# Optimization experiments

Hardware: AMD Instinct MI355X
Metric: run time of the kernel (lower is better)

Reference implementation:

```python
import jax, jax.numpy as jnp
import numpy as np

B, S, D, H, O = 8, 4096, 512, 512, 512
NS, NC, SD = 4, 4, 8
CLIP, TEMP, SUP_SCALE, SUP_EPS, LN_EPS = 3.0, 1.0, 1.0, 1e-4, 1e-5


def _ln(x, w, b):
    m = jnp.mean(x, -1, keepdims=True)
    v = jnp.mean((x - m) ** 2, -1, keepdims=True)
    return (x - m) * jax.lax.rsqrt(v + LN_EPS) * w + b


def _lin(x, w, b):
    return x @ w.T + b


def setup_inputs() -> dict:
    key = jax.random.key(0)
    ks = iter(jax.random.split(key, 32))

    def W(shape):
        return 0.02 * jax.random.normal(next(ks), shape, jnp.float32)

    inp = {}
    inp['x'] = jax.random.normal(next(ks), (B, S, D), jnp.float32)
    inp['sb_norm_w'] = jnp.ones((D,), jnp.float32)
    inp['sb_norm_b'] = jnp.zeros((D,), jnp.float32)
    inp['sb_proj_w'] = W((NS, D)); inp['sb_proj_b'] = jnp.zeros((NS,), jnp.float32)
    inp['sb_sum_w'] = W((SD, 4)); inp['sb_sum_b'] = jnp.zeros((SD,), jnp.float32)
    inp['cb_norm_w'] = jnp.ones((D,), jnp.float32)
    inp['cb_norm_b'] = jnp.zeros((D,), jnp.float32)
    inp['cb_proj_w'] = W((NC, D)); inp['cb_proj_b'] = jnp.zeros((NC,), jnp.float32)
    inp['cb_sum_w'] = W((SD, 4)); inp['cb_sum_b'] = jnp.zeros((SD,), jnp.float32)
    inp['vn_norm_w'] = jnp.ones((D,), jnp.float32)
    inp['vn_norm_b'] = jnp.zeros((D,), jnp.float32)
    inp['vn_w1'] = W((H, D)); inp['vn_b1'] = jnp.zeros((H,), jnp.float32)
    inp['vn_w2'] = W((O, H)); inp['vn_b2'] = jnp.zeros((O,), jnp.float32)
    inp['un_norm_w'] = jnp.ones((D,), jnp.float32)
    inp['un_norm_b'] = jnp.zeros((D,), jnp.float32)
    inp['un_w1'] = W((H, D)); inp['un_b1'] = jnp.zeros((H,), jnp.float32)
    inp['un_w2'] = W((1, H)); inp['un_b2'] = jnp.zeros((1,), jnp.float32)
    inp['en_w'] = W((H, 1)); inp['en_b'] = jnp.zeros((H,), jnp.float32)
    inp['pr_w'] = W((H, 1)); inp['pr_b'] = jnp.zeros((H,), jnp.float32)
    inp['rs_w'] = W((H, 1)); inp['rs_b'] = jnp.zeros((H,), jnp.float32)
    inp['ssp_w'] = W((H, SD)); inp['ssp_b'] = jnp.zeros((H,), jnp.float32)
    inp['csp_w'] = W((H, SD)); inp['csp_b'] = jnp.zeros((H,), jnp.float32)
    inp['out_w'] = W((O, O + 5 * H)); inp['out_b'] = jnp.zeros((O,), jnp.float32)
    inp['support_logits'] = jnp.zeros((NS,), jnp.float32)
    inp['conflict_weights'] = jnp.ones((NC,), jnp.float32)
    inp['drive_bias'] = jnp.zeros((1,), jnp.float32)
    inp['bias_resistance'] = jnp.zeros((1,), jnp.float32)
    inp['update_threshold'] = jnp.ones((1,), jnp.float32)
    inp['eml_gamma'] = jnp.full((1,), 0.3, jnp.float32)
    inp['eml_lambda'] = jnp.ones((1,), jnp.float32)
    inp['eml_bias'] = jnp.zeros((1,), jnp.float32)
    return inp


def reference(x, sb_norm_w, sb_norm_b, sb_proj_w, sb_proj_b, sb_sum_w, sb_sum_b,
              cb_norm_w, cb_norm_b, cb_proj_w, cb_proj_b, cb_sum_w, cb_sum_b,
              vn_norm_w, vn_norm_b, vn_w1, vn_b1, vn_w2, vn_b2,
              un_norm_w, un_norm_b, un_w1, un_b1, un_w2, un_b2,
              en_w, en_b, pr_w, pr_b, rs_w, rs_b,
              ssp_w, ssp_b, csp_w, csp_b, out_w, out_b,
              support_logits, conflict_weights, drive_bias, bias_resistance,
              update_threshold, eml_gamma, eml_lambda, eml_bias):
    # Support bank: LN -> Linear -> softplus(+eps) -> stats -> summary Linear
    sf = jax.nn.softplus(_lin(_ln(x, sb_norm_w, sb_norm_b), sb_proj_w, sb_proj_b)) + SUP_EPS  # [B,S,NS]
    ls = jnp.log(sf)
    s_seed = jnp.concatenate([
        sf.mean(-1, keepdims=True), sf.std(-1, keepdims=True),
        ls.mean(-1, keepdims=True), ls.max(-1, keepdims=True)], -1)
    ss = _lin(s_seed, sb_sum_w, sb_sum_b)  # [B,S,SD]
    # Conflict bank
    cf = jax.nn.softplus(_lin(_ln(x, cb_norm_w, cb_norm_b), cb_proj_w, cb_proj_b))  # [B,S,NC]
    c_seed = jnp.concatenate([
        cf.mean(-1, keepdims=True), cf.std(-1, keepdims=True),
        cf.max(-1, keepdims=True), cf.min(-1, keepdims=True)], -1)
    cs = _lin(c_seed, cb_sum_w, cb_sum_b)  # [B,S,SD]
    # Drive / resistance
    sw = jax.nn.softmax(support_logits)
    drive = drive_bias + SUP_SCALE * (ls * sw).sum(-1, keepdims=True) / np.sqrt(NS)
    cw = jax.nn.softplus(conflict_weights)
    weighted_conflict = (cf * cw).sum(-1, keepdims=True) / np.sqrt(NC)
    u_h = jax.nn.gelu(_lin(_ln(x, un_norm_w, un_norm_b), un_w1, un_b1), approximate=False)
    uncertainty = jax.nn.softplus(_lin(u_h, un_w2, un_b2))  # [B,S,1]
    resistance = bias_resistance + weighted_conflict + uncertainty
    # EML unit (dim=1): bounded linear drive-resistance balance, warmup_eta=1.0
    e_raw = eml_gamma * drive - eml_lambda * resistance + eml_bias
    energy = CLIP * jnp.tanh(e_raw / CLIP)
    activation = jax.nn.sigmoid(energy / TEMP)
    precision = jax.nn.softplus(energy - update_threshold)
    # Value net
    v_h = jax.nn.gelu(_lin(_ln(x, vn_norm_w, vn_norm_b), vn_w1, vn_b1), approximate=False)
    value = _lin(v_h, vn_w2, vn_b2)  # [B,S,O]
    feats = jnp.concatenate([
        activation * value,
        _lin(energy, en_w, en_b),
        _lin(precision, pr_w, pr_b),
        _lin(resistance, rs_w, rs_b),
        _lin(ss, ssp_w, ssp_b),
        _lin(cs, csp_w, csp_b)], -1)  # [B,S,O+5H]
    return _lin(feats, out_w, out_b)  # [B,S,O]
```

## Files before the change

kernel.cpp:

```cpp
#include <hip/hip_runtime.h>
#include <stdint.h>

typedef unsigned short u16;
typedef __bf16 bf16x8 __attribute__((ext_vector_type(8)));
typedef float f32x4 __attribute__((ext_vector_type(4)));
typedef __attribute__((address_space(1))) void gvoid;
typedef __attribute__((address_space(3))) void lvoid;

#define NTOK 32768

__device__ __forceinline__ u16 f2bf(float f) {
    unsigned u = __float_as_uint(f);
    u += 0x7fffu + ((u >> 16) & 1u);
    return (u16)(u >> 16);
}
__device__ __forceinline__ float softplusf(float x) {
    return fmaxf(x, 0.f) + log1pf(expf(-fabsf(x)));
}
__device__ __forceinline__ float geluf(float x) {
    return 0.5f * x * (1.f + erff(x * 0.7071067811865475f));
}
__device__ __forceinline__ float wave_sum(float v) {
#pragma unroll
    for (int o = 32; o > 0; o >>= 1) v += __shfl_xor(v, o);
    return v;
}
__device__ __forceinline__ float blk_sum(float v) {
    __shared__ float sm[4];
    v = wave_sum(v);
    __syncthreads();
    if ((threadIdx.x & 63) == 0) sm[threadIdx.x >> 6] = v;
    __syncthreads();
    return sm[0] + sm[1] + sm[2] + sm[3];
}

__global__ void k_fold(
    const float* __restrict__ vnw1, const float* __restrict__ vnnw, const float* __restrict__ vnnb, const float* __restrict__ vnb1,
    const float* __restrict__ unw1, const float* __restrict__ unnw, const float* __restrict__ unnb, const float* __restrict__ unb1,
    const float* __restrict__ sbpw, const float* __restrict__ sbpb, const float* __restrict__ sbnw, const float* __restrict__ sbnb,
    const float* __restrict__ cbpw, const float* __restrict__ cbpb, const float* __restrict__ cbnw, const float* __restrict__ cbnb,
    const float* __restrict__ outw, const float* __restrict__ enw, const float* __restrict__ enb,
    const float* __restrict__ prw, const float* __restrict__ prb,
    const float* __restrict__ rsw, const float* __restrict__ rsb,
    const float* __restrict__ sspw, const float* __restrict__ sspb,
    const float* __restrict__ cspw, const float* __restrict__ cspb,
    const float* __restrict__ vnw2, const float* __restrict__ vnb2,
    u16* __restrict__ Astk, float* __restrict__ bstk, float* __restrict__ pb,
    u16* __restrict__ Aow, u16* __restrict__ vnT,
    float* __restrict__ a_en, float* __restrict__ a_pr, float* __restrict__ a_rs,
    float* __restrict__ b_vo, float* __restrict__ c_cn, float* __restrict__ Mss, float* __restrict__ Mcs)
{
    const int b = blockIdx.x, t = threadIdx.x;
    if (b < 1024) {
        const float *w1, *nw, *nb; float bias;
        if (b < 512) { w1 = vnw1 + (size_t)b * 512; nw = vnnw; nb = vnnb; bias = vnb1[b]; }
        else { int r = b - 512; w1 = unw1 + (size_t)r * 512; nw = unnw; nb = unnb; bias = unb1[r]; }
        float part = 0.f;
        for (int d = t; d < 512; d += 256) {
            float wv = w1[d];
            Astk[(size_t)b * 512 + d] = f2bf(wv * nw[d]);
            part += wv * nb[d];
        }
        float s = blk_sum(part);
        if (t == 0) bstk[b] = bias + s;
    } else if (b < 1032) {
        int j = b - 1024;
        const float *pw, *nw, *nb; float bias;
        if (j < 4) { pw = sbpw + j * 512; nw = sbnw; nb = sbnb; bias = sbpb[j]; }
        else { pw = cbpw + (j - 4) * 512; nw = cbnw; nb = cbnb; bias = cbpb[j - 4]; }
        float part = 0.f;
        for (int d = t; d < 512; d += 256) {
            float wv = pw[d];
            Astk[(size_t)(1024 + j) * 512 + d] = f2bf(wv * nw[d]);
            part += wv * nb[d];
        }
        float s = blk_sum(part);
        if (t == 0) pb[j] = bias + s;
    } else if (b < 1152) {
        for (int d = t; d < 512; d += 256) Astk[(size_t)b * 512 + d] = 0;
    } else if (b < 1664) {
        int i = b - 1152;
        const float* ow = outw + (size_t)i * 3072;
        float pen = 0, ppr = 0, prs = 0, pbv = 0, pcc = 0;
        float pms[8], pmc[8];
#pragma unroll
        for (int k = 0; k < 8; k++) { pms[k] = 0.f; pmc[k] = 0.f; }
        for (int h = t; h < 512; h += 256) {
            float o0 = ow[h];        Aow[(size_t)i * 512 + h] = f2bf(o0); pbv += o0 * vnb2[h];
            float o1 = ow[512 + h];  pen += o1 * enw[h]; pcc += o1 * enb[h];
            float o2 = ow[1024 + h]; ppr += o2 * prw[h]; pcc += o2 * prb[h];
            float o3 = ow[1536 + h]; prs += o3 * rsw[h]; pcc += o3 * rsb[h];
            float o4 = ow[2048 + h]; pcc += o4 * sspb[h];
            float o5 = ow[2560 + h]; pcc += o5 * cspb[h];
#pragma unroll
            for (int k = 0; k < 8; k++) { pms[k] += o4 * sspw[h * 8 + k]; pmc[k] += o5 * cspw[h * 8 + k]; }
        }
        float r;
        r = blk_sum(pen); if (t == 0) a_en[i] = r;
        r = blk_sum(ppr); if (t == 0) a_pr[i] = r;
        r = blk_sum(prs); if (t == 0) a_rs[i] = r;
        r = blk_sum(pbv); if (t == 0) b_vo[i] = r;
        r = blk_sum(pcc); if (t == 0) c_cn[i] = r;
        for (int k = 0; k < 8; k++) { r = blk_sum(pms[k]); if (t == 0) Mss[i * 8 + k] = r; }
        for (int k = 0; k < 8; k++) { r = blk_sum(pmc[k]); if (t == 0) Mcs[i * 8 + k] = r; }
    } else {
        int hrow = b - 1664;
        for (int o = t; o < 512; o += 256)
            vnT[(size_t)hrow * 512 + o] = f2bf(vnw2[(size_t)o * 512 + hrow]);
    }
}

__device__ __forceinline__ void gt_stage(const u16* __restrict__ A_, int lda,
                                         const u16* __restrict__ B_, int ldb, int kt,
                                         u16* dA, u16* dB, int w, int lrow, int lcol)
{
#pragma unroll
    for (int i = 0; i < 4; i++) {
        const int chunk = i * 4 + w;
        const int row = chunk * 8 + lrow;
        __builtin_amdgcn_global_load_lds((gvoid*)const_cast<u16*>(A_ + (size_t)row * lda + kt + lcol),
                                         (lvoid*)(dA + chunk * 512), 16, 0, 0);
        __builtin_amdgcn_global_load_lds((gvoid*)const_cast<u16*>(B_ + (size_t)row * ldb + kt + lcol),
                                         (lvoid*)(dB + chunk * 512), 16, 0, 0);
    }
}

__device__ __forceinline__ void gt_compute(const u16* lA, const u16* lB, f32x4 (&acc)[4][4],
                                           int wr, int wc, int frow, int fk, int sw)
{
#pragma unroll
    for (int ks = 0; ks < 2; ks++) {
        bf16x8 af[4], bfv[4];
        const int c = (ks * 32 + fk);
#pragma unroll
        for (int rt = 0; rt < 4; rt++)
            af[rt] = *(const bf16x8*)(lA + (wr + rt * 16 + frow) * 64 + (c ^ sw));
#pragma unroll
        for (int ct = 0; ct < 4; ct++)
            bfv[ct] = *(const bf16x8*)(lB + (wc + ct * 16 + frow) * 64 + (c ^ sw));
#pragma unroll
        for (int rt = 0; rt < 4; rt++)
#pragma unroll
            for (int ct = 0; ct < 4; ct++)
                acc[rt][ct] = __builtin_amdgcn_mfma_f32_16x16x32_bf16(af[rt], bfv[ct], acc[rt][ct], 0, 0, 0);
    }
}

__device__ __forceinline__ void gemm_tile(const u16* __restrict__ Ab, int lda,
                                          const u16* __restrict__ Bb, int ldb,
                                          int K, u16* sm, f32x4 (&acc)[4][4])
{
    const int t = threadIdx.x;
    const int w = t >> 6, l = t & 63;
    const int lrow = l >> 3;
    const int lcol = ((l ^ (((l >> 3) & 3) << 1)) & 7) * 8;
    const int wr = ((w >> 1) << 6), wc = ((w & 1) << 6);
    const int frow = l & 15, fk = ((l >> 4) << 3);
    const int sw = (frow & 3) << 4;
    u16* lA0 = sm;          u16* lA1 = sm + 8192;
    u16* lB0 = sm + 16384;  u16* lB1 = sm + 24576;

    gt_stage(Ab, lda, Bb, ldb, 0, lA0, lB0, w, lrow, lcol);
    __syncthreads();
    for (int kt = 0; kt < K; kt += 128) {
        if (kt + 64 < K) gt_stage(Ab, lda, Bb, ldb, kt + 64, lA1, lB1, w, lrow, lcol);
        gt_compute(lA0, lB0, acc, wr, wc, frow, fk, sw);
        __syncthreads();
        if (kt + 128 < K) gt_stage(Ab, lda, Bb, ldb, kt + 128, lA0, lB0, w, lrow, lcol);
        gt_compute(lA1, lB1, acc, wr, wc, frow, fk, sw);
        __syncthreads();
    }
}

__global__ __launch_bounds__(256, 2) void k_gemm_wvo(const u16* __restrict__ A, const u16* __restrict__ Bm,
                                                     u16* __restrict__ C)
{
    __shared__ __align__(16) u16 smem[32768];
    const f32x4 zero = {0.f, 0.f, 0.f, 0.f};
    f32x4 acc[4][4];
#pragma unroll
    for (int a = 0; a < 4; a++)
#pragma unroll
        for (int c = 0; c < 4; c++) acc[a][c] = zero;
    const u16* Ab = A + (size_t)blockIdx.y * 128 * 512;
    const u16* Bb = Bm + (size_t)blockIdx.x * 128 * 512;
    gemm_tile(Ab, 512, Bb, 512, 512, smem, acc);
    const int t = threadIdx.x, w = t >> 6, l = t & 63;
    const int rbase = blockIdx.y * 128 + ((w >> 1) << 6);
    const int cbase = blockIdx.x * 128 + ((w & 1) << 6);
    const int lr = ((l >> 4) << 2), lc = l & 15;
#pragma unroll
    for (int rt = 0; rt < 4; rt++)
#pragma unroll
        for (int ct = 0; ct < 4; ct++)
#pragma unroll
            for (int j = 0; j < 4; j++)
                C[(size_t)(rbase + rt * 16 + lr + j) * 512 + cbase + ct * 16 + lc] = f2bf(acc[rt][ct][j]);
}

__global__ void k_token(const float* __restrict__ x, u16* __restrict__ Ybf)
{
    const int w = threadIdx.x >> 6, l = threadIdx.x & 63;
    const int n = blockIdx.x * 4 + w;
    const float* xr = x + (size_t)n * 512;
    float4 xa = *(const float4*)(xr + 4 * l);
    float4 xb = *(const float4*)(xr + 256 + 4 * l);
    float v[8] = {xa.x, xa.y, xa.z, xa.w, xb.x, xb.y, xb.z, xb.w};
    float s1 = 0.f, s2 = 0.f;
#pragma unroll
    for (int c = 0; c < 8; c++) { s1 += v[c]; s2 += v[c] * v[c]; }
    s1 = wave_sum(s1); s2 = wave_sum(s2);
    const float mean = s1 * (1.f / 512.f);
    const float var = s2 * (1.f / 512.f) - mean * mean;
    const float rstd = rsqrtf(var + 1e-5f);
    float y[8];
#pragma unroll
    for (int c = 0; c < 8; c++) y[c] = (v[c] - mean) * rstd;
    *(ushort4*)(Ybf + (size_t)n * 512 + 4 * l) = make_ushort4(f2bf(y[0]), f2bf(y[1]), f2bf(y[2]), f2bf(y[3]));
    *(ushort4*)(Ybf + (size_t)n * 512 + 256 + 4 * l) = make_ushort4(f2bf(y[4]), f2bf(y[5]), f2bf(y[6]), f2bf(y[7]));
}

__global__ __launch_bounds__(256, 2) void k_gemm1(const u16* __restrict__ Y, const u16* __restrict__ Ast,
                                                  const float* __restrict__ bstk, const float* __restrict__ pb,
                                                  const float* __restrict__ unw2,
                                                  u16* __restrict__ H, float* __restrict__ wp,
                                                  float* __restrict__ wdotp)
{
    __shared__ __align__(16) u16 smem[32768];
    const f32x4 zero = {0.f, 0.f, 0.f, 0.f};
    f32x4 acc[4][4];
#pragma unroll
    for (int a = 0; a < 4; a++)
#pragma unroll
        for (int c = 0; c < 4; c++) acc[a][c] = zero;
    const int nwg = gridDim.x * gridDim.y;
    const int lin = blockIdx.y * gridDim.x + blockIdx.x;
    const int swz = (lin & 7) * (nwg >> 3) + (lin >> 3);
    const int by = swz / gridDim.x, bx = swz % gridDim.x;
    const u16* Ab = Y + (size_t)by * 128 * 512;
    const u16* Bb = Ast + (size_t)bx * 128 * 512;
    gemm_tile(Ab, 512, Bb, 512, 512, smem, acc);
    const int t = threadIdx.x, w = t >> 6, l = t & 63;
    const int wr = ((w >> 1) << 6), wc = ((w & 1) << 6);
    const int lr = ((l >> 4) << 2), lc = l & 15;
    if (bx == 8) {
        if ((w & 1) == 0 && lc < 8) {
            const float bv = pb[lc];
            const int rbase = by * 128 + wr;
#pragma unroll
            for (int rt = 0; rt < 4; rt++)
#pragma unroll
                for (int j = 0; j < 4; j++) {
                    const int n = rbase + rt * 16 + lr + j;
                    wp[(size_t)n * 8 + lc] = acc[rt][0][j] + bv;
                }
        }
        return;
    }
    if (bx >= 4) {
        const int cb = (bx - 4) * 128;
        float part[4][4];
#pragma unroll
        for (int rt = 0; rt < 4; rt++)
#pragma unroll
            for (int j = 0; j < 4; j++) part[rt][j] = 0.f;
#pragma unroll
        for (int ct = 0; ct < 4; ct++) {
            const int col = cb + wc + ct * 16 + lc;
            const float bv = bstk[512 + col];
            const float w2 = unw2[col];
#pragma unroll
            for (int rt = 0; rt < 4; rt++)
#pragma unroll
                for (int j = 0; j < 4; j++)
                    part[rt][j] += geluf(acc[rt][ct][j] + bv) * w2;
        }
        float* sf = (float*)smem;
        const int slot = ((w & 1) << 4) | lc;
        __syncthreads();
#pragma unroll
        for (int rt = 0; rt < 4; rt++)
#pragma unroll
            for (int j = 0; j < 4; j++)
                sf[(wr + rt * 16 + lr + j) * 32 + slot] = part[rt][j];
        __syncthreads();
        if (t < 128) {
            float s = 0.f;
#pragma unroll
            for (int k2 = 0; k2 < 32; k2++) s += sf[t * 32 + k2];
            wdotp[(size_t)(bx - 4) * NTOK + by * 128 + t] = s;
        }
        return;
    }
#pragma unroll
    for (int ct = 0; ct < 4; ct++) {
        const int col = wc + ct * 16 + lc;
        const float bv = bstk[bx * 128 + col];
#pragma unroll
        for (int rt = 0; rt < 4; rt++) {
            const int row = wr + rt * 16 + lr;
#pragma unroll
            for (int j = 0; j < 4; j++)
                smem[(row + j) * 136 + col] = f2bf(geluf(acc[rt][ct][j] + bv));
        }
    }
    __syncthreads();
    const size_t gbase = (size_t)(by * 128) * 512 + bx * 128;
#pragma unroll
    for (int jj = 0; jj < 8; jj++) {
        const int r = jj * 16 + (t >> 4), u = t & 15;
        bf16x8 vv = *(const bf16x8*)(smem + r * 136 + u * 8);
        *(bf16x8*)(H + gbase + (size_t)r * 512 + u * 8) = vv;
    }
}

__global__ void k_bank(const float* __restrict__ wp, const float* __restrict__ wdotp,
                       const float* __restrict__ unb2,
                       const float* __restrict__ sbsw, const float* __restrict__ sbsb,
                       const float* __restrict__ cbsw, const float* __restrict__ cbsb,
                       const float* __restrict__ suplog, const float* __restrict__ confw,
                       const float* __restrict__ drvb, const float* __restrict__ biasres,
                       const float* __restrict__ emlg, const float* __restrict__ emll,
                       const float* __restrict__ emlb, const float* __restrict__ updthr,
                       float* __restrict__ wss, float* __restrict__ wcs, float* __restrict__ wsc)
{
    const int n = blockIdx.x * 256 + threadIdx.x;
    float4 p0 = *(const float4*)(wp + (size_t)n * 8);
    float4 p1 = *(const float4*)(wp + (size_t)n * 8 + 4);
    float p[8] = {p0.x, p0.y, p0.z, p0.w, p1.x, p1.y, p1.z, p1.w};
    const float dot = wdotp[n] + wdotp[NTOK + n] + wdotp[2 * NTOK + n] + wdotp[3 * NTOK + n];
    float sf[4], lsv[4], cf[4];
#pragma unroll
    for (int j = 0; j < 4; j++) {
        sf[j] = softplusf(p[j]) + 1e-4f;
        lsv[j] = logf(sf[j]);
        cf[j] = softplusf(p[j + 4]);
    }
    const float smn = 0.25f * (sf[0] + sf[1] + sf[2] + sf[3]);
    float sd = 0.f;
#pragma unroll
    for (int j = 0; j < 4; j++) sd += (sf[j] - smn) * (sf[j] - smn);
    const float sstd = sqrtf(0.25f * sd);
    const float lmn = 0.25f * (lsv[0] + lsv[1] + lsv[2] + lsv[3]);
    const float lmx = fmaxf(fmaxf(lsv[0], lsv[1]), fmaxf(lsv[2], lsv[3]));
    const float cmn = 0.25f * (cf[0] + cf[1] + cf[2] + cf[3]);
    float cd = 0.f;
#pragma unroll
    for (int j = 0; j < 4; j++) cd += (cf[j] - cmn) * (cf[j] - cmn);
    const float cstd = sqrtf(0.25f * cd);
    const float cmx = fmaxf(fmaxf(cf[0], cf[1]), fmaxf(cf[2], cf[3]));
    const float cmi = fminf(fminf(cf[0], cf[1]), fminf(cf[2], cf[3]));
    float seed_s[4] = {smn, sstd, lmn, lmx};
    float seed_c[4] = {cmn, cstd, cmx, cmi};
    float a4[8], b4[8];
#pragma unroll
    for (int k = 0; k < 8; k++) {
        float a = sbsb[k], b2 = cbsb[k];
#pragma unroll
        for (int j = 0; j < 4; j++) { a += sbsw[k * 4 + j] * seed_s[j]; b2 += cbsw[k * 4 + j] * seed_c[j]; }
        a4[k] = a; b4[k] = b2;
    }
    *(float4*)(wss + (size_t)n * 8)     = make_float4(a4[0], a4[1], a4[2], a4[3]);
    *(float4*)(wss + (size_t)n * 8 + 4) = make_float4(a4[4], a4[5], a4[6], a4[7]);
    *(float4*)(wcs + (size_t)n * 8)     = make_float4(b4[0], b4[1], b4[2], b4[3]);
    *(float4*)(wcs + (size_t)n * 8 + 4) = make_float4(b4[4], b4[5], b4[6], b4[7]);
    float mx = fmaxf(fmaxf(suplog[0], suplog[1]), fmaxf(suplog[2], suplog[3]));
    float e[4], se = 0.f;
#pragma unroll
    for (int j = 0; j < 4; j++) { e[j] = expf(suplog[j] - mx); se += e[j]; }
    float dv = 0.f, wcv = 0.f;
#pragma unroll
    for (int j = 0; j < 4; j++) { dv += lsv[j] * (e[j] / se); wcv += cf[j] * softplusf(confw[j]); }
    const float drive = drvb[0] + 0.5f * dv;
    const float unc = softplusf(dot + unb2[0]);
    const float res = biasres[0] + 0.5f * wcv + unc;
    const float er = emlg[0] * drive - emll[0] * res + emlb[0];
    const float energy = 3.f * tanhf(er * (1.f / 3.f));
    const float act = 1.f / (1.f + expf(-energy));
    const float prc = softplusf(energy - updthr[0]);
    wsc[(size_t)n * 4 + 0] = act;
    wsc[(size_t)n * 4 + 1] = energy;
    wsc[(size_t)n * 4 + 2] = prc;
    wsc[(size_t)n * 4 + 3] = res;
}

__global__ __launch_bounds__(256, 2) void k_gemm2(const u16* __restrict__ H, const u16* __restrict__ Wvo,
    const float* __restrict__ wsc, const float* __restrict__ wss, const float* __restrict__ wcs,
    const float* __restrict__ a_en, const float* __restrict__ a_pr, const float* __restrict__ a_rs,
    const float* __restrict__ b_vo, const float* __restrict__ c_cn,
    const float* __restrict__ Mss, const float* __restrict__ Mcs,
    const float* __restrict__ outb, float* __restrict__ out)
{
    __shared__ __align__(16) u16 smem[32768];
    const f32x4 zero = {0.f, 0.f, 0.f, 0.f};
    f32x4 acc[4][4];
#pragma unroll
    for (int a = 0; a < 4; a++)
#pragma unroll
        for (int c = 0; c < 4; c++) acc[a][c] = zero;
    const int nwg = gridDim.x * gridDim.y;
    const int lin = blockIdx.y * gridDim.x + blockIdx.x;
    const int swz = (lin & 7) * (nwg >> 3) + (lin >> 3);
    const int by = swz / gridDim.x, bx = swz % gridDim.x;
    const u16* Ab = H + (size_t)by * 128 * 512;
    const u16* Bb = Wvo + (size_t)bx * 128 * 512;
    gemm_tile(Ab, 512, Bb, 512, 512, smem, acc);
    const int t = threadIdx.x, w = t >> 6, l = t & 63;
    const int rbase = by * 128 + ((w >> 1) << 6);
    const int cbase = bx * 128 + ((w & 1) << 6);
    const int lr = ((l >> 4) << 2), lc = l & 15;
    float bvo4[4], aen4[4], apr4[4], ars4[4], cc4[4], ms4[4][8], mc4[4][8];
#pragma unroll
    for (int ct = 0; ct < 4; ct++) {
        const int i = cbase + ct * 16 + lc;
        bvo4[ct] = b_vo[i]; aen4[ct] = a_en[i]; apr4[ct] = a_pr[i]; ars4[ct] = a_rs[i];
        cc4[ct] = c_cn[i] + outb[i];
#pragma unroll
        for (int k = 0; k < 8; k++) { ms4[ct][k] = Mss[i * 8 + k]; mc4[ct][k] = Mcs[i * 8 + k]; }
    }
#pragma unroll
    for (int rt = 0; rt < 4; rt++)
#pragma unroll
        for (int j = 0; j < 4; j++) {
            const int n = rbase + rt * 16 + lr + j;
            const float act = wsc[(size_t)n * 4 + 0];
            const float eng = wsc[(size_t)n * 4 + 1];
            const float prc = wsc[(size_t)n * 4 + 2];
            const float res = wsc[(size_t)n * 4 + 3];
            float sv[8], cv[8];
#pragma unroll
            for (int k = 0; k < 8; k++) { sv[k] = wss[(size_t)n * 8 + k]; cv[k] = wcs[(size_t)n * 8 + k]; }
#pragma unroll
            for (int ct = 0; ct < 4; ct++) {
                const int i = cbase + ct * 16 + lc;
                float o = act * (acc[rt][ct][j] + bvo4[ct]) + eng * aen4[ct] + prc * apr4[ct]
                        + res * ars4[ct] + cc4[ct];
#pragma unroll
                for (int k = 0; k < 8; k++) o += ms4[ct][k] * sv[k] + mc4[ct][k] * cv[k];
                out[(size_t)n * 512 + i] = o;
            }
        }
}

extern "C" void kernel_launch(void* const* d_in, const int* in_sizes, int n_in,
                              void* d_out, int out_size, void* d_ws, size_t ws_size,
                              hipStream_t stream)
{
    const float* x       = (const float*)d_in[0];
    const float* sbnw    = (const float*)d_in[1];
    const float* sbnb    = (const float*)d_in[2];
    const float* sbpw    = (const float*)d_in[3];
    const float* sbpb    = (const float*)d_in[4];
    const float* sbsw    = (const float*)d_in[5];
    const float* sbsb    = (const float*)d_in[6];
    const float* cbnw    = (const float*)d_in[7];
    const float* cbnb    = (const float*)d_in[8];
    const float* cbpw    = (const float*)d_in[9];
    const float* cbpb    = (const float*)d_in[10];
    const float* cbsw    = (const float*)d_in[11];
    const float* cbsb    = (const float*)d_in[12];
    const float* vnnw    = (const float*)d_in[13];
    const float* vnnb    = (const float*)d_in[14];
    const float* vnw1    = (const float*)d_in[15];
    const float* vnb1    = (const float*)d_in[16];
    const float* vnw2    = (const float*)d_in[17];
    const float* vnb2    = (const float*)d_in[18];
    const float* unnw    = (const float*)d_in[19];
    const float* unnb    = (const float*)d_in[20];
    const float* unw1    = (const float*)d_in[21];
    const float* unb1    = (const float*)d_in[22];
    const float* unw2    = (const float*)d_in[23];
    const float* unb2    = (const float*)d_in[24];
    const float* enw     = (const float*)d_in[25];
    const float* enb     = (const float*)d_in[26];
    const float* prw     = (const float*)d_in[27];
    const float* prb     = (const float*)d_in[28];
    const float* rsw     = (const float*)d_in[29];
    const float* rsb     = (const float*)d_in[30];
    const float* sspw    = (const float*)d_in[31];
    const float* sspb    = (const float*)d_in[32];
    const float* cspw    = (const float*)d_in[33];
    const float* cspb    = (const float*)d_in[34];
    const float* outw    = (const float*)d_in[35];
    const float* outb    = (const float*)d_in[36];
    const float* suplog  = (const float*)d_in[37];
    const float* confw   = (const float*)d_in[38];
    const float* drvb    = (const float*)d_in[39];
    const float* biasres = (const float*)d_in[40];
    const float* updthr  = (const float*)d_in[41];
    const float* emlg    = (const float*)d_in[42];
    const float* emll    = (const float*)d_in[43];
    const float* emlb    = (const float*)d_in[44];
    float* out = (float*)d_out;
    (void)in_sizes; (void)n_in; (void)out_size; (void)ws_size;

    char* wsp = (char*)d_ws;
    size_t off = 0;
    auto alloc = [&](size_t bytes) { char* p = wsp + off; off = (off + bytes + 255) & ~(size_t)255; return p; };
    u16*  Ybf  = (u16*)alloc((size_t)NTOK * 512 * 2);
    u16*  Hbf  = (u16*)alloc((size_t)NTOK * 512 * 2);
    u16*  Astk = (u16*)alloc(1152 * 512 * 2);
    float* bstk = (float*)alloc(1024 * 4);
    float* pb   = (float*)alloc(8 * 4);
    u16*  Aow  = (u16*)alloc(512 * 512 * 2);
    u16*  vnT  = (u16*)alloc(512 * 512 * 2);
    u16*  Wvo  = (u16*)alloc(512 * 512 * 2);
    float* a_en = (float*)alloc(512 * 4);
    float* a_pr = (float*)alloc(512 * 4);
    float* a_rs = (float*)alloc(512 * 4);
    float* b_vo = (float*)alloc(512 * 4);
    float* c_cn = (float*)alloc(512 * 4);
    float* Mss  = (float*)alloc(512 * 8 * 4);
    float* Mcs  = (float*)alloc(512 * 8 * 4);
    float* wp   = (float*)alloc((size_t)NTOK * 8 * 4);
    float* wdotp= (float*)alloc((size_t)NTOK * 4 * 4);
    float* wss  = (float*)alloc((size_t)NTOK * 8 * 4);
    float* wcs  = (float*)alloc((size_t)NTOK * 8 * 4);
    float* wsc  = (float*)alloc((size_t)NTOK * 4 * 4);

    k_fold<<<2176, 256, 0, stream>>>(vnw1, vnnw, vnnb, vnb1, unw1, unnw, unnb, unb1,
                                     sbpw, sbpb, sbnw, sbnb, cbpw, cbpb, cbnw, cbnb,
                                     outw, enw, enb, prw, prb, rsw, rsb, sspw, sspb, cspw, cspb,
                                     vnw2, vnb2,
                                     Astk, bstk, pb, Aow, vnT, a_en, a_pr, a_rs, b_vo, c_cn, Mss, Mcs);
    k_gemm_wvo<<<dim3(4, 4), 256, 0, stream>>>(Aow, vnT, Wvo);
    k_token<<<NTOK / 4, 256, 0, stream>>>(x, Ybf);
    k_gemm1<<<dim3(9, 256), 256, 0, stream>>>(Ybf, Astk, bstk, pb, unw2, Hbf, wp, wdotp);
    k_bank<<<NTOK / 256, 256, 0, stream>>>(wp, wdotp, unb2, sbsw, sbsb, cbsw, cbsb,
                                           suplog, confw, drvb, biasres, emlg, emll, emlb, updthr,
                                           wss, wcs, wsc);
    k_gemm2<<<dim3(4, 256), 256, 0, stream>>>(Hbf, Wvo, wsc, wss, wcs, a_en, a_pr, a_rs, b_vo, c_cn,
                                              Mss, Mcs, outb, out);
}
```

Before: 154.9 us.

## Switch GEMMs to 256x256 tiles with 8-wave pipelined mainloop

Replaces the 128x128, 4-wave GEMM tiles in k_gemm1 and k_gemm2 with 256x256 tiles computed by 512-thread blocks. A new mainloop issues staged global-to-LDS loads split by quadrant, with explicit vmcnt waits, barriers and raised wave priority around the MFMA bursts. The stacked weight matrix is padded to 1280 rows so the bank projection fits in a fifth tile column, and the uncertainty partial dot shrinks from four partials to two. Larger tiles cut redundant global loads and raise arithmetic intensity, but they need 128KB of LDS and many accumulator registers, leave fewer blocks, and waste padded rows in the bank tile.

Result: slower. 530.1 us (+242.3%).

```diff
diff --git a/kernel.cpp b/kernel.cpp
--- a/kernel.cpp
+++ b/kernel.cpp
@@ -8,6 +8,11 @@
 typedef __attribute__((address_space(3))) void lvoid;
 
 #define NTOK 32768
+
+#define FENCE() asm volatile("" ::: "memory")
+#define SBAR()  do { FENCE(); __builtin_amdgcn_s_barrier(); FENCE(); } while (0)
+#define SVM6()  asm volatile("s_waitcnt vmcnt(6)" ::: "memory")
+#define SVM0()  asm volatile("s_waitcnt vmcnt(0)" ::: "memory")
 
 __device__ __forceinline__ u16 f2bf(float f) {
     unsigned u = __float_as_uint(f);
@@ -76,10 +81,10 @@
         }
         float s = blk_sum(part);
         if (t == 0) pb[j] = bias + s;
-    } else if (b < 1152) {
+    } else if (b < 1280) {
         for (int d = t; d < 512; d += 256) Astk[(size_t)b * 512 + d] = 0;
-    } else if (b < 1664) {
-        int i = b - 1152;
+    } else if (b < 1792) {
+        int i = b - 1280;
         const float* ow = outw + (size_t)i * 3072;
         float pen = 0, ppr = 0, prs = 0, pbv = 0, pcc = 0;
         float pms[8], pmc[8];
@@ -104,9 +109,109 @@
         for (int k = 0; k < 8; k++) { r = blk_sum(pms[k]); if (t == 0) Mss[i * 8 + k] = r; }
         for (int k = 0; k < 8; k++) { r = blk_sum(pmc[k]); if (t == 0) Mcs[i * 8 + k] = r; }
     } else {
-        int hrow = b - 1664;
+        int hrow = b - 1792;
         for (int o = t; o < 512; o += 256)
             vnT[(size_t)hrow * 512 + o] = f2bf(vnw2[(size_t)o * 512 + hrow]);
+    }
+}
+
+__device__ __forceinline__ void load_bfrag(const u16* bufB, bf16x8 (&bfrag)[4][2], int wn, int l) {
+#pragma unroll
+    for (int nt = 0; nt < 4; nt++) {
+        const int row = wn * 64 + nt * 16 + (l & 15);
+#pragma unroll
+        for (int ks = 0; ks < 2; ks++) {
+            const int s = (ks * 4 + (l >> 4)) ^ (row & 7);
+            bfrag[nt][ks] = *(const bf16x8*)(bufB + row * 64 + (s << 3));
+        }
+    }
+}
+
+template <int Q>
+__device__ __forceinline__ void load_aquad(const u16* bufA, bf16x8 (&af)[2][2], int wm, int l) {
+#pragma unroll
+    for (int m2 = 0; m2 < 2; m2++) {
+        const int row = (Q * 2 + m2) * 32 + wm * 16 + (l & 15);
+#pragma unroll
+        for (int ks = 0; ks < 2; ks++) {
+            const int s = (ks * 4 + (l >> 4)) ^ (row & 7);
+            af[m2][ks] = *(const bf16x8*)(bufA + row * 64 + (s << 3));
+        }
+    }
+}
+
+template <int Q>
+__device__ __forceinline__ void do_mfma(bf16x8 (&af)[2][2], bf16x8 (&bfrag)[4][2], f32x4 (&acc)[8][4]) {
+#pragma unroll
+    for (int m2 = 0; m2 < 2; m2++)
+#pragma unroll
+        for (int nt = 0; nt < 4; nt++)
+#pragma unroll
+            for (int ks = 0; ks < 2; ks++)
+                acc[Q * 2 + m2][nt] =
+                    __builtin_amdgcn_mfma_f32_16x16x32_bf16(af[m2][ks], bfrag[nt][ks], acc[Q * 2 + m2][nt], 0, 0, 0);
+}
+
+#define PHASE(Q, bufA_, bufB_, READB, STAGE_STMT, VM_STMT)        \
+    do {                                                          \
+        if (READB) load_bfrag(bufB_, bfrag, wn, l);               \
+        bf16x8 af[2][2];                                          \
+        load_aquad<Q>(bufA_, af, wm, l);                          \
+        STAGE_STMT;                                               \
+        SBAR();                                                   \
+        __builtin_amdgcn_s_setprio(1);                            \
+        do_mfma<Q>(af, bfrag, acc);                               \
+        __builtin_amdgcn_s_setprio(0);                            \
+        VM_STMT;                                                  \
+        SBAR();                                                   \
+    } while (0)
+
+__device__ __forceinline__ void gemm8_mainloop(const u16* __restrict__ Ag, const u16* __restrict__ Bg,
+                                               size_t arow0, size_t brow0,
+                                               u16* sm, f32x4 (&acc)[8][4], int w, int l)
+{
+    const int wm = w >> 2, wn = w & 3;
+    u16* const sA0 = sm;
+    u16* const sA1 = sm + 16384;
+    u16* const sB0 = sm + 32768;
+    u16* const sB1 = sm + 49152;
+    const int rchunk = l >> 3;
+    const int gc = (((l & 7) ^ (l >> 3)) << 3);
+
+    auto STG = [&](const u16* g, size_t rb, int tile, int half, u16* lbase) {
+        const int kt = tile * 64;
+#pragma unroll
+        for (int i = 0; i < 2; i++) {
+            const int r0 = half * 128 + (w * 2 + i) * 8;
+            __builtin_amdgcn_global_load_lds(
+                (gvoid*)const_cast<u16*>(g + (rb + r0 + rchunk) * 512 + kt + gc),
+                (lvoid*)(lbase + r0 * 64), 16, 0, 0);
+        }
+    };
+
+    STG(Ag, arow0, 0, 0, sA0);
+    STG(Ag, arow0, 0, 1, sA0);
+    STG(Bg, brow0, 0, 0, sB0);
+    STG(Bg, brow0, 0, 1, sB0);
+    STG(Bg, brow0, 1, 0, sB1);
+    STG(Ag, arow0, 1, 0, sA1);
+    STG(Bg, brow0, 1, 1, sB1);
+    SVM6();
+    SBAR();
+
+    bf16x8 bfrag[4][2];
+    for (int it = 0; it < 4; ++it) {
+        const int t1 = 2 * it + 1, t2 = 2 * it + 2, t3 = 2 * it + 3;
+        const bool lastit = (it == 3);
+        PHASE(0, sA0, sB0, true,  { STG(Ag, arow0, t1, 1, sA1); }, );
+        PHASE(1, sA0, sB0, false, { if (t2 < 8) STG(Bg, brow0, t2, 0, sB0); }, );
+        PHASE(2, sA0, sB0, false, { if (t2 < 8) STG(Ag, arow0, t2, 0, sA0); }, );
+        PHASE(3, sA0, sB0, false, { if (t2 < 8) STG(Bg, brow0, t2, 1, sB0); },
+              { if (lastit) { SVM0(); } else { SVM6(); } });
+        PHASE(0, sA1, sB1, true,  { if (t2 < 8) STG(Ag, arow0, t2, 1, sA0); }, );
+        PHASE(1, sA1, sB1, false, { if (t3 < 8) STG(Bg, brow0, t3, 0, sB1); }, );
+        PHASE(2, sA1, sB1, false, { if (t3 < 8) STG(Ag, arow0, t3, 0, sA1); }, );
+        PHASE(3, sA1, sB1, false, { if (t3 < 8) STG(Bg, brow0, t3, 1, sB1); }, { SVM6(); });
     }
 }
 
@@ -124,7 +229,6 @@
                                          (lvoid*)(dB + chunk * 512), 16, 0, 0);
     }
 }
-
 __device__ __forceinline__ void gt_compute(const u16* lA, const u16* lB, f32x4 (&acc)[4][4],
                                            int wr, int wc, int frow, int fk, int sw)
 {
@@ -145,7 +249,6 @@
                 acc[rt][ct] = __builtin_amdgcn_mfma_f32_16x16x32_bf16(af[rt], bfv[ct], acc[rt][ct], 0, 0, 0);
     }
 }
-
 __device__ __forceinline__ void gemm_tile(const u16* __restrict__ Ab, int lda,
                                           const u16* __restrict__ Bb, int ldb,
                                           int K, u16* sm, f32x4 (&acc)[4][4])
@@ -159,7 +262,6 @@
     const int sw = (frow & 3) << 4;
     u16* lA0 = sm;          u16* lA1 = sm + 8192;
     u16* lB0 = sm + 16384;  u16* lB1 = sm + 24576;
-
     gt_stage(Ab, lda, Bb, ldb, 0, lA0, lB0, w, lrow, lcol);
     __syncthreads();
     for (int kt = 0; kt < K; kt += 128) {
@@ -220,97 +322,90 @@
     *(ushort4*)(Ybf + (size_t)n * 512 + 256 + 4 * l) = make_ushort4(f2bf(y[4]), f2bf(y[5]), f2bf(y[6]), f2bf(y[7]));
 }
 
-__global__ __launch_bounds__(256, 2) void k_gemm1(const u16* __restrict__ Y, const u16* __restrict__ Ast,
+__global__ __launch_bounds__(512, 2) void k_gemm1(const u16* __restrict__ Y, const u16* __restrict__ Ast,
                                                   const float* __restrict__ bstk, const float* __restrict__ pb,
                                                   const float* __restrict__ unw2,
                                                   u16* __restrict__ H, float* __restrict__ wp,
                                                   float* __restrict__ wdotp)
 {
-    __shared__ __align__(16) u16 smem[32768];
-    const f32x4 zero = {0.f, 0.f, 0.f, 0.f};
-    f32x4 acc[4][4];
-#pragma unroll
-    for (int a = 0; a < 4; a++)
-#pragma unroll
-        for (int c = 0; c < 4; c++) acc[a][c] = zero;
+    __shared__ __align__(16) u16 smem[65536];
+    f32x4 acc[8][4];
+#pragma unroll
+    for (int a = 0; a < 8; a++)
+#pragma unroll
+        for (int c = 0; c < 4; c++) acc[a][c] = (f32x4){0.f, 0.f, 0.f, 0.f};
     const int nwg = gridDim.x * gridDim.y;
     const int lin = blockIdx.y * gridDim.x + blockIdx.x;
     const int swz = (lin & 7) * (nwg >> 3) + (lin >> 3);
     const int by = swz / gridDim.x, bx = swz % gridDim.x;
-    const u16* Ab = Y + (size_t)by * 128 * 512;
-    const u16* Bb = Ast + (size_t)bx * 128 * 512;
-    gemm_tile(Ab, 512, Bb, 512, 512, smem, acc);
-    const int t = threadIdx.x, w = t >> 6, l = t & 63;
-    const int wr = ((w >> 1) << 6), wc = ((w & 1) << 6);
-    const int lr = ((l >> 4) << 2), lc = l & 15;
-    if (bx == 8) {
-        if ((w & 1) == 0 && lc < 8) {
-            const float bv = pb[lc];
-            const int rbase = by * 128 + wr;
-#pragma unroll
-            for (int rt = 0; rt < 4; rt++)
+    const int tid = threadIdx.x, w = tid >> 6, l = tid & 63;
+    const int wm = w >> 2, wn = w & 3;
+
+    gemm8_mainloop(Y, Ast, (size_t)by * 256, (size_t)bx * 256, smem, acc, w, l);
+
+    if (bx >= 4) {
+        if (wn == 0 && (l & 15) < 8) {
+            const float bv = pb[l & 15];
+#pragma unroll
+            for (int mt = 0; mt < 8; mt++)
 #pragma unroll
                 for (int j = 0; j < 4; j++) {
-                    const int n = rbase + rt * 16 + lr + j;
-                    wp[(size_t)n * 8 + lc] = acc[rt][0][j] + bv;
+                    const int n = by * 256 + mt * 32 + wm * 16 + ((l >> 4) << 2) + j;
+                    wp[(size_t)n * 8 + (l & 15)] = acc[mt][0][j] + bv;
                 }
         }
         return;
     }
-    if (bx >= 4) {
-        const int cb = (bx - 4) * 128;
-        float part[4][4];
-#pragma unroll
-        for (int rt = 0; rt < 4; rt++)
-#pragma unroll
-            for (int j = 0; j < 4; j++) part[rt][j] = 0.f;
-#pragma unroll
-        for (int ct = 0; ct < 4; ct++) {
-            const int col = cb + wc + ct * 16 + lc;
-            const float bv = bstk[512 + col];
-            const float w2 = unw2[col];
-#pragma unroll
-            for (int rt = 0; rt < 4; rt++)
-#pragma unroll
-                for (int j = 0; j < 4; j++)
-                    part[rt][j] += geluf(acc[rt][ct][j] + bv) * w2;
-        }
+    if (bx >= 2) {
         float* sf = (float*)smem;
-        const int slot = ((w & 1) << 4) | lc;
+#pragma unroll
+        for (int mt = 0; mt < 8; mt++)
+#pragma unroll
+            for (int j = 0; j < 4; j++) {
+                float ps = 0.f;
+#pragma unroll
+                for (int nt = 0; nt < 4; nt++) {
+                    const int c = wn * 64 + nt * 16 + (l & 15);
+                    const int ui = (bx - 2) * 256 + c;
+                    ps += geluf(acc[mt][nt][j] + bstk[512 + ui]) * unw2[ui];
+                }
+                const int row = mt * 32 + wm * 16 + ((l >> 4) << 2) + j;
+                sf[row * 65 + wn * 16 + (l & 15)] = ps;
+            }
         __syncthreads();
-#pragma unroll
-        for (int rt = 0; rt < 4; rt++)
-#pragma unroll
-            for (int j = 0; j < 4; j++)
-                sf[(wr + rt * 16 + lr + j) * 32 + slot] = part[rt][j];
+        if (tid < 256) {
+            float s = 0.f;
+#pragma unroll
+            for (int c = 0; c < 64; c++) s += sf[tid * 65 + c];
+            wdotp[(size_t)(bx - 2) * NTOK + by * 256 + tid] = s;
+        }
+        return;
+    }
+#pragma unroll
+    for (int p = 0; p < 2; p++) {
+#pragma unroll
+        for (int m2 = 0; m2 < 4; m2++) {
+            const int mt = p * 4 + m2;
+#pragma unroll
+            for (int nt = 0; nt < 4; nt++) {
+                const int c = wn * 64 + nt * 16 + (l & 15);
+                const float bv = bstk[bx * 256 + c];
+#pragma unroll
+                for (int j = 0; j < 4; j++) {
+                    const int rloc = mt * 32 + wm * 16 + ((l >> 4) << 2) + j - p * 128;
+                    smem[rloc * 264 + c] = f2bf(geluf(acc[mt][nt][j] + bv));
+                }
+            }
+        }
         __syncthreads();
-        if (t < 128) {
-            float s = 0.f;
-#pragma unroll
-            for (int k2 = 0; k2 < 32; k2++) s += sf[t * 32 + k2];
-            wdotp[(size_t)(bx - 4) * NTOK + by * 128 + t] = s;
-        }
-        return;
-    }
-#pragma unroll
-    for (int ct = 0; ct < 4; ct++) {
-        const int col = wc + ct * 16 + lc;
-        const float bv = bstk[bx * 128 + col];
-#pragma unroll
-        for (int rt = 0; rt < 4; rt++) {
-            const int row = wr + rt * 16 + lr;
-#pragma unroll
-            for (int j = 0; j < 4; j++)
-                smem[(row + j) * 136 + col] = f2bf(geluf(acc[rt][ct][j] + bv));
-        }
-    }
-    __syncthreads();
-    const size_t gbase = (size_t)(by * 128) * 512 + bx * 128;
-#pragma unroll
-    for (int jj = 0; jj < 8; jj++) {
-        const int r = jj * 16 + (t >> 4), u = t & 15;
-        bf16x8 vv = *(const bf16x8*)(smem + r * 136 + u * 8);
-        *(bf16x8*)(H + gbase + (size_t)r * 512 + u * 8) = vv;
+        const int r = tid >> 5, u = tid & 31;
+#pragma unroll
+        for (int s = 0; s < 8; s++) {
+            const int rr = s * 16 + r;
+            bf16x8 vv = *(const bf16x8*)(smem + rr * 264 + u * 8);
+            *(bf16x8*)(H + (size_t)(by * 256 + p * 128 + rr) * 512 + bx * 256 + u * 8) = vv;
+        }
+        __syncthreads();
     }
 }
 
@@ -328,7 +423,7 @@
     float4 p0 = *(const float4*)(wp + (size_t)n * 8);
     float4 p1 = *(const float4*)(wp + (size_t)n * 8 + 4);
     float p[8] = {p0.x, p0.y, p0.z, p0.w, p1.x, p1.y, p1.z, p1.w};
-    const float dot = wdotp[n] + wdotp[NTOK + n] + wdotp[2 * NTOK + n] + wdotp[3 * NTOK + n];
+    const float dot = wdotp[n] + wdotp[NTOK + n];
     float sf[4], lsv[4], cf[4];
 #pragma unroll
     for (int j = 0; j < 4; j++) {
@@ -384,62 +479,66 @@
     wsc[(size_t)n * 4 + 3] = res;
 }
 
-__global__ __launch_bounds__(256, 2) void k_gemm2(const u16* __restrict__ H, const u16* __restrict__ Wvo,
+__global__ __launch_bounds__(512, 2) void k_gemm2(const u16* __restrict__ H, const u16* __restrict__ Wvo,
     const float* __restrict__ wsc, const float* __restrict__ wss, const float* __restrict__ wcs,
     const float* __restrict__ a_en, const float* __restrict__ a_pr, const float* __restrict__ a_rs,
     const float* __restrict__ b_vo, const float* __restrict__ c_cn,
     const float* __restrict__ Mss, const float* __restrict__ Mcs,
     const float* __restrict__ outb, float* __restrict__ out)
 {
-    __shared__ __align__(16) u16 smem[32768];
-    const f32x4 zero = {0.f, 0.f, 0.f, 0.f};
-    f32x4 acc[4][4];
-#pragma unroll
-    for (int a = 0; a < 4; a++)
-#pragma unroll
-        for (int c = 0; c < 4; c++) acc[a][c] = zero;
+    __shared__ __align__(16) u16 smem[65536];
+    f32x4 acc[8][4];
+#pragma unroll
+    for (int a = 0; a < 8; a++)
+#pragma unroll
+        for (int c = 0; c < 4; c++) acc[a][c] = (f32x4){0.f, 0.f, 0.f, 0.f};
     const int nwg = gridDim.x * gridDim.y;
     const int lin = blockIdx.y * gridDim.x + blockIdx.x;
     const int swz = (lin & 7) * (nwg >> 3) + (lin >> 3);
     const int by = swz / gridDim.x, bx = swz % gridDim.x;
-    const u16* Ab = H + (size_t)by * 128 * 512;
-    const u16* Bb = Wvo + (size_t)bx * 128 * 512;
-    gemm_tile(Ab, 512, Bb, 512, 512, smem, acc);
-    const int t = threadIdx.x, w = t >> 6, l = t & 63;
-    const int rbase = by * 128 + ((w >> 1) << 6);
-    const int cbase = bx * 128 + ((w & 1) << 6);
-    const int lr = ((l >> 4) << 2), lc = l & 15;
-    float bvo4[4], aen4[4], apr4[4], ars4[4], cc4[4], ms4[4][8], mc4[4][8];
-#pragma unroll
-    for (int ct = 0; ct < 4; ct++) {
-        const int i = cbase + ct * 16 + lc;
-        bvo4[ct] = b_vo[i]; aen4[ct] = a_en[i]; apr4[ct] = a_pr[i]; ars4[ct] = a_rs[i];
-        cc4[ct] = c_cn[i] + outb[i];
-#pragma unroll
-        for (int k = 0; k < 8; k++) { ms4[ct][k] = Mss[i * 8 + k]; mc4[ct][k] = Mcs[i * 8 + k]; }
-    }
-#pragma unroll
-    for (int rt = 0; rt < 4; rt++)
-#pragma unroll
-        for (int j = 0; j < 4; j++) {
-            const int n = rbase + rt * 16 + lr + j;
-            const float act = wsc[(size_t)n * 4 + 0];
-            const float eng = wsc[(size_t)n * 4 + 1];
-            const float prc = wsc[(size_t)n * 4 + 2];
-            const float res = wsc[(size_t)n * 4 + 3];
-            float sv[8], cv[8];
-#pragma unroll
-            for (int k = 0; k < 8; k++) { sv[k] = wss[(size_t)n * 8 + k]; cv[k] = wcs[(size_t)n * 8 + k]; }
-#pragma unroll
-            for (int ct = 0; ct < 4; ct++) {
-                const int i = cbase + ct * 16 + lc;
-                float o = act * (acc[rt][ct][j] + bvo4[ct]) + eng * aen4[ct] + prc * apr4[ct]
-                        + res * ars4[ct] + cc4[ct];
-#pragma unroll
-                for (int k = 0; k < 8; k++) o += ms4[ct][k] * sv[k] + mc4[ct][k] * cv[k];
-                out[(size_t)n * 512 + i] = o;
+    const int tid = threadIdx.x, w = tid >> 6, l = tid & 63;
+    const int wm = w >> 2, wn = w & 3;
+
+    gemm8_mainloop(H, Wvo, (size_t)by * 256, (size_t)bx * 256, smem, acc, w, l);
+
+#pragma unroll
+    for (int h = 0; h < 2; h++) {
+        float bvo2[2], aen2[2], apr2[2], ars2[2], cc2[2], ms2[2][8], mc2[2][8];
+#pragma unroll
+        for (int u2 = 0; u2 < 2; u2++) {
+            const int i = bx * 256 + wn * 64 + (h * 2 + u2) * 16 + (l & 15);
+            bvo2[u2] = b_vo[i]; aen2[u2] = a_en[i]; apr2[u2] = a_pr[i]; ars2[u2] = a_rs[i];
+            cc2[u2] = c_cn[i] + outb[i];
+#pragma unroll
+            for (int k = 0; k < 8; k++) { ms2[u2][k] = Mss[i * 8 + k]; mc2[u2][k] = Mcs[i * 8 + k]; }
+        }
+#pragma unroll
+        for (int mt = 0; mt < 8; mt++)
+#pragma unroll
+            for (int j = 0; j < 4; j++) {
+                const size_t n = (size_t)by * 256 + mt * 32 + wm * 16 + ((l >> 4) << 2) + j;
+                const float act = wsc[n * 4 + 0];
+                const float eng = wsc[n * 4 + 1];
+                const float prc = wsc[n * 4 + 2];
+                const float res = wsc[n * 4 + 3];
+                float o[2];
+#pragma unroll
+                for (int u2 = 0; u2 < 2; u2++)
+                    o[u2] = act * (acc[mt][h * 2 + u2][j] + bvo2[u2]) + eng * aen2[u2]
+                          + prc * apr2[u2] + res * ars2[u2] + cc2[u2];
+#pragma unroll
+                for (int k = 0; k < 8; k++) {
+                    const float sv = wss[n * 8 + k], cv = wcs[n * 8 + k];
+#pragma unroll
+                    for (int u2 = 0; u2 < 2; u2++) o[u2] += ms2[u2][k] * sv + mc2[u2][k] * cv;
+                }
+#pragma unroll
+                for (int u2 = 0; u2 < 2; u2++) {
+                    const int i = bx * 256 + wn * 64 + (h * 2 + u2) * 16 + (l & 15);
+                    out[n * 512 + i] = o[u2];
+                }
             }
-        }
+    }
 }
 
 extern "C" void kernel_launch(void* const* d_in, const int* in_sizes, int n_in,
@@ -499,7 +598,7 @@
     auto alloc = [&](size_t bytes) { char* p = wsp + off; off = (off + bytes + 255) & ~(size_t)255; return p; };
     u16*  Ybf  = (u16*)alloc((size_t)NTOK * 512 * 2);
     u16*  Hbf  = (u16*)alloc((size_t)NTOK * 512 * 2);
-    u16*  Astk = (u16*)alloc(1152 * 512 * 2);
+    u16*  Astk = (u16*)alloc(1280 * 512 * 2);
     float* bstk = (float*)alloc(1024 * 4);
     float* pb   = (float*)alloc(8 * 4);
     u16*  Aow  = (u16*)alloc(512 * 512 * 2);
@@ -513,22 +612,22 @@
     float* Mss  = (float*)alloc(512 * 8 * 4);
     float* Mcs  = (float*)alloc(512 * 8 * 4);
     float* wp   = (float*)alloc((size_t)NTOK * 8 * 4);
-    float* wdotp= (float*)alloc((size_t)NTOK * 4 * 4);
+    float* wdotp= (float*)alloc((size_t)NTOK * 2 * 4);
     float* wss  = (float*)alloc((size_t)NTOK * 8 * 4);
     float* wcs  = (float*)alloc((size_t)NTOK * 8 * 4);
     float* wsc  = (float*)alloc((size_t)NTOK * 4 * 4);
 
-    k_fold<<<2176, 256, 0, stream>>>(vnw1, vnnw, vnnb, vnb1, unw1, unnw, unnb, unb1,
+    k_fold<<<2304, 256, 0, stream>>>(vnw1, vnnw, vnnb, vnb1, unw1, unnw, unnb, unb1,
                                      sbpw, sbpb, sbnw, sbnb, cbpw, cbpb, cbnw, cbnb,
                                      outw, enw, enb, prw, prb, rsw, rsb, sspw, sspb, cspw, cspb,
                                      vnw2, vnb2,
                                      Astk, bstk, pb, Aow, vnT, a_en, a_pr, a_rs, b_vo, c_cn, Mss, Mcs);
     k_gemm_wvo<<<dim3(4, 4), 256, 0, stream>>>(Aow, vnT, Wvo);
     k_token<<<NTOK / 4, 256, 0, stream>>>(x, Ybf);
-    k_gemm1<<<dim3(9, 256), 256, 0, stream>>>(Ybf, Astk, bstk, pb, unw2, Hbf, wp, wdotp);
+    k_gemm1<<<dim3(5, 128), 512, 0, stream>>>(Ybf, Astk, bstk, pb, unw2, Hbf, wp, wdotp);
     k_bank<<<NTOK / 256, 256, 0, stream>>>(wp, wdotp, unb2, sbsw, sbsb, cbsw, cbsb,
                                            suplog, confw, drvb, biasres, emlg, emll, emlb, updthr,
                                            wss, wcs, wsc);
-    k_gemm2<<<dim3(4, 256), 256, 0, stream>>>(Hbf, Wvo, wsc, wss, wcs, a_en, a_pr, a_rs, b_vo, c_cn,
+    k_gemm2<<<dim3(2, 128), 512, 0, stream>>>(Hbf, Wvo, wsc, wss, wcs, a_en, a_pr, a_rs, b_vo, c_cn,
                                               Mss, Mcs, outb, out);
 }
```

## Replace GEMM main loop with eight-phase barrier-interleaved pipeline in both GEMMs

Applied to the files above, without the earlier changes.

Adds a new GEMM main loop that splits each 64-wide K tile into four phases, one per 16-row A quad. Each phase interleaves LDS fragment reads, async global-to-LDS staging and MFMA bursts, using explicit s_barrier, vmcnt waits and s_setprio. Both k_gemm1 and k_gemm2 switch to it, and a new XOR swizzle across all 8 row slots replaces the old swizzle. The aim is to hide global-load latency and LDS bank conflicts behind MFMA work, at the cost of many more barriers per tile and fragile hand-set vmcnt counts.

Measured after the change: 154.1 us. No clear change (-0.5%).

```diff
diff --git a/kernel.cpp b/kernel.cpp
--- a/kernel.cpp
+++ b/kernel.cpp
@@ -8,6 +8,11 @@
 typedef __attribute__((address_space(3))) void lvoid;
 
 #define NTOK 32768
+
+#define FENCE() asm volatile("" ::: "memory")
+#define SBAR()  do { FENCE(); __builtin_amdgcn_s_barrier(); FENCE(); } while (0)
+#define SVM4()  asm volatile("s_waitcnt vmcnt(4)" ::: "memory")
+#define SVM0()  asm volatile("s_waitcnt vmcnt(0)" ::: "memory")
 
 __device__ __forceinline__ u16 f2bf(float f) {
     unsigned u = __float_as_uint(f);
@@ -110,6 +115,95 @@
     }
 }
 
+__device__ __forceinline__ void load_bfrag8(const u16* bufB, bf16x8 (&bfrag)[4][2], int wn, int l) {
+#pragma unroll
+    for (int nt = 0; nt < 4; nt++) {
+        const int row = wn * 64 + nt * 16 + (l & 15);
+#pragma unroll
+        for (int ks = 0; ks < 2; ks++) {
+            const int s = (ks * 4 + (l >> 4)) ^ (row & 7);
+            bfrag[nt][ks] = *(const bf16x8*)(bufB + row * 64 + (s << 3));
+        }
+    }
+}
+
+template <int Q>
+__device__ __forceinline__ void load_aquad8(const u16* bufA, bf16x8 (&af)[2], int wm, int l) {
+    const int row = wm * 64 + Q * 16 + (l & 15);
+#pragma unroll
+    for (int ks = 0; ks < 2; ks++) {
+        const int s = (ks * 4 + (l >> 4)) ^ (row & 7);
+        af[ks] = *(const bf16x8*)(bufA + row * 64 + (s << 3));
+    }
+}
+
+template <int Q>
+__device__ __forceinline__ void do_mfma8(bf16x8 (&af)[2], bf16x8 (&bfrag)[4][2], f32x4 (&acc)[4][4]) {
+#pragma unroll
+    for (int nt = 0; nt < 4; nt++)
+#pragma unroll
+        for (int ks = 0; ks < 2; ks++)
+            acc[Q][nt] = __builtin_amdgcn_mfma_f32_16x16x32_bf16(af[ks], bfrag[nt][ks], acc[Q][nt], 0, 0, 0);
+}
+
+#define PHASE8(Q, bufA_, bufB_, READB, STAGE_STMT, VM_STMT)       \
+    do {                                                          \
+        if (READB) load_bfrag8(bufB_, bfrag, wn, l);              \
+        bf16x8 af[2];                                             \
+        load_aquad8<Q>(bufA_, af, wm, l);                         \
+        STAGE_STMT;                                               \
+        SBAR();                                                   \
+        __builtin_amdgcn_s_setprio(1);                            \
+        do_mfma8<Q>(af, bfrag, acc);                              \
+        __builtin_amdgcn_s_setprio(0);                            \
+        VM_STMT;                                                  \
+        SBAR();                                                   \
+    } while (0)
+
+__device__ __forceinline__ void gemm8_mainloop(const u16* __restrict__ Ag, const u16* __restrict__ Bg,
+                                               size_t arow0, size_t brow0,
+                                               u16* sm, f32x4 (&acc)[4][4], int w, int l)
+{
+    const int wm = w >> 1, wn = w & 1;
+    u16* const sA0 = sm;
+    u16* const sA1 = sm + 8192;
+    u16* const sB0 = sm + 16384;
+    u16* const sB1 = sm + 24576;
+    const int rchunk = l >> 3;
+    const int gc = (((l & 7) ^ ((l >> 3) & 7)) << 3);
+
+    auto STG = [&](const u16* g, size_t rb, int tile, u16* lbase) {
+        const int kt = tile * 64;
+#pragma unroll
+        for (int i = 0; i < 4; i++) {
+            const int r0 = (w * 4 + i) * 8;
+            __builtin_amdgcn_global_load_lds(
+                (gvoid*)const_cast<u16*>(g + (rb + r0 + rchunk) * 512 + kt + gc),
+                (lvoid*)(lbase + r0 * 64), 16, 0, 0);
+        }
+    };
+
+    STG(Ag, arow0, 0, sA0);
+    STG(Bg, brow0, 0, sB0);
+    STG(Bg, brow0, 1, sB1);
+    SVM4();
+    SBAR();
+
+    bf16x8 bfrag[4][2];
+    for (int it = 0; it < 4; ++it) {
+        const int t1 = 2 * it + 1, t2 = 2 * it + 2, t3 = 2 * it + 3;
+        const bool lastit = (it == 3);
+        PHASE8(0, sA0, sB0, true,  { STG(Ag, arow0, t1, sA1); }, );
+        PHASE8(1, sA0, sB0, false, { if (t2 < 8) STG(Bg, brow0, t2, sB0); }, );
+        PHASE8(2, sA0, sB0, false, { }, );
+        PHASE8(3, sA0, sB0, false, { }, { if (lastit) { SVM0(); } else { SVM4(); } });
+        PHASE8(0, sA1, sB1, true,  { if (t2 < 8) STG(Ag, arow0, t2, sA0); }, );
+        PHASE8(1, sA1, sB1, false, { if (t3 < 8) STG(Bg, brow0, t3, sB1); }, );
+        PHASE8(2, sA1, sB1, false, { }, );
+        PHASE8(3, sA1, sB1, false, { }, { SVM4(); });
+    }
+}
+
 __device__ __forceinline__ void gt_stage(const u16* __restrict__ A_, int lda,
                                          const u16* __restrict__ B_, int ldb, int kt,
                                          u16* dA, u16* dB, int w, int lrow, int lcol)
@@ -124,7 +218,6 @@
                                          (lvoid*)(dB + chunk * 512), 16, 0, 0);
     }
 }
-
 __device__ __forceinline__ void gt_compute(const u16* lA, const u16* lB, f32x4 (&acc)[4][4],
                                            int wr, int wc, int frow, int fk, int sw)
 {
@@ -145,7 +238,6 @@
                 acc[rt][ct] = __builtin_amdgcn_mfma_f32_16x16x32_bf16(af[rt], bfv[ct], acc[rt][ct], 0, 0, 0);
     }
 }
-
 __device__ __forceinline__ void gemm_tile(const u16* __restrict__ Ab, int lda,
                                           const u16* __restrict__ Bb, int ldb,
                                           int K, u16* sm, f32x4 (&acc)[4][4])
@@ -159,7 +251,6 @@
     const int sw = (frow & 3) << 4;
     u16* lA0 = sm;          u16* lA1 = sm + 8192;
     u16* lB0 = sm + 16384;  u16* lB1 = sm + 24576;
-
     gt_stage(Ab, lda, Bb, ldb, 0, lA0, lB0, w, lrow, lcol);
     __syncthreads();
     for (int kt = 0; kt < K; kt += 128) {
@@ -237,10 +328,10 @@
     const int lin = blockIdx.y * gridDim.x + blockIdx.x;
     const int swz = (lin & 7) * (nwg >> 3) + (lin >> 3);
     const int by = swz / gridDim.x, bx = swz % gridDim.x;
-    const u16* Ab = Y + (size_t)by * 128 * 512;
-    const u16* Bb = Ast + (size_t)bx * 128 * 512;
-    gemm_tile(Ab, 512, Bb, 512, 512, smem, acc);
     const int t = threadIdx.x, w = t >> 6, l = t & 63;
+
+    gemm8_mainloop(Y, Ast, (size_t)by * 128, (size_t)bx * 128, smem, acc, w, l);
+
     const int wr = ((w >> 1) << 6), wc = ((w & 1) << 6);
     const int lr = ((l >> 4) << 2), lc = l & 15;
     if (bx == 8) {
@@ -292,6 +383,7 @@
         }
         return;
     }
+    __syncthreads();
 #pragma unroll
     for (int ct = 0; ct < 4; ct++) {
         const int col = wc + ct * 16 + lc;
@@ -402,10 +494,10 @@
     const int lin = blockIdx.y * gridDim.x + blockIdx.x;
     const int swz = (lin & 7) * (nwg >> 3) + (lin >> 3);
     const int by = swz / gridDim.x, bx = swz % gridDim.x;
-    const u16* Ab = H + (size_t)by * 128 * 512;
-    const u16* Bb = Wvo + (size_t)bx * 128 * 512;
-    gemm_tile(Ab, 512, Bb, 512, 512, smem, acc);
     const int t = threadIdx.x, w = t >> 6, l = t & 63;
+
+    gemm8_mainloop(H, Wvo, (size_t)by * 128, (size_t)bx * 128, smem, acc, w, l);
+
     const int rbase = by * 128 + ((w >> 1) << 6);
     const int cbase = bx * 128 + ((w & 1) << 6);
     const int lr = ((l >> 4) << 2), lc = l & 15;
```
